# Kernel tuning notes

Hardware: AMD Instinct MI355X
Metric: run time of the kernel (lower is better)

## Reference

```python
import jax, jax.numpy as jnp
from jax import lax
import numpy as np

HEADS = 8
SR = 4  # sr_ratio
LN_EPS = 1e-5


def gaussian_filt(x, kernel_size, sigma):
    # depthwise gaussian blur, x: [B, C, H, W]
    ch = x.shape[1]
    c = jnp.arange(kernel_size, dtype=x.dtype)
    xx = jnp.broadcast_to(c[None, :], (kernel_size, kernel_size))
    yy = xx.T
    mean = (kernel_size - 1) / 2.0
    g = jnp.exp(-((xx - mean) ** 2 + (yy - mean) ** 2) / (2.0 * sigma * sigma))
    g = g / g.sum()  # normalization cancels the 1/(2*pi*var) factor
    kern = jnp.broadcast_to(g[None, None], (ch, 1, kernel_size, kernel_size)).astype(x.dtype)
    p = (kernel_size - 1) // 2
    return lax.conv_general_dilated(
        x, kern, (1, 1), [(p, p), (p, p)],
        dimension_numbers=('NCHW', 'OIHW', 'NCHW'), feature_group_count=ch)


def reconstruct_feature(feature, mask, kernel_size, sigma):
    if kernel_size <= 1:
        return feature
    feature = feature * mask
    out = gaussian_filt(jnp.concatenate([feature, mask], axis=1), kernel_size, sigma)
    f_int = out[:, :-1]
    m_int = out[:, -1:]
    f_int = f_int / (m_int + 1e-6)
    m_bin = (m_int > 0).astype(feature.dtype)
    f_int = f_int * m_bin
    return feature + (1.0 - mask) * f_int


def token2map(x, loc, H, W, kernel_size, sigma):
    # x: [B, N, C], loc: [B, N, 2] in [0,1]
    B, N, C = x.shape
    loc = jnp.clip(loc, 0.0, 1.0) * jnp.array([W - 1, H - 1], dtype=loc.dtype)
    loc = jnp.round(loc).astype(jnp.int32)
    idx = loc[..., 0] + loc[..., 1] * W + (jnp.arange(B, dtype=jnp.int32) * (H * W))[:, None]
    src = jnp.concatenate([x, jnp.ones((B, N, 1), x.dtype)], axis=-1).reshape(B * N, C + 1)
    out = jax.ops.segment_sum(src, idx.reshape(-1), num_segments=B * H * W)
    out = out.reshape(B, H, W, C + 1).transpose(0, 3, 1, 2)  # [B, C+1, H, W]
    feature, mask = out[:, :-1], out[:, -1:]
    feature = feature / (mask + 1e-6)
    mask = (mask > 0).astype(x.dtype)
    feature = feature * mask
    return reconstruct_feature(feature, mask, kernel_size, sigma)


def layer_norm(x, w, b):
    mu = jnp.mean(x, axis=-1, keepdims=True)
    var = jnp.mean((x - mu) ** 2, axis=-1, keepdims=True)
    return (x - mu) * lax.rsqrt(var + LN_EPS) * w + b


def forward(x, x_source, loc_source, conf_source, Wq, Wk, Wv, sr_w, sr_b, ln_w, ln_b, Wp, bp, H, W):
    B, N, C = x.shape
    dh = C // HEADS
    scale = dh ** -0.5
    q = (x @ Wq.T).reshape(B, N, HEADS, dh).transpose(0, 2, 1, 3)  # [B,h,N,dh]
    # token2map + spatial reduction
    xm = token2map(x_source, loc_source, H, W, SR - 1, 2.0)        # [B,C,H,W]
    xs = lax.conv_general_dilated(
        xm, sr_w, (SR, SR), 'VALID',
        dimension_numbers=('NCHW', 'OIHW', 'NCHW')) + sr_b[None, :, None, None]
    xs = xs.reshape(B, C, -1).transpose(0, 2, 1)                   # [B,Ns,C]
    xs = layer_norm(xs, ln_w, ln_b)
    Ns = xs.shape[1]
    k = (xs @ Wk.T).reshape(B, Ns, HEADS, dh).transpose(0, 2, 1, 3)
    v = (xs @ Wv.T).reshape(B, Ns, HEADS, dh).transpose(0, 2, 1, 3)
    attn = jnp.einsum('bhnd,bhmd->bhnm', q, k) * scale             # [B,h,N,Ns]
    attn = attn + conf_source[..., 0][:, None, None, :]            # additive bias
    attn = jax.nn.softmax(attn, axis=-1)
    out = jnp.einsum('bhnm,bhmd->bhnd', attn, v)
    out = out.transpose(0, 2, 1, 3).reshape(B, N, C)
    return out @ Wp.T + bp


def setup_inputs() -> dict:
    key = jax.random.key(0)
    ks = jax.random.split(key, 10)
    B, N, C, Hm = 2, 8192, 256, 128
    Ns = (Hm // SR) * (Hm // SR)
    s = 0.02
    return {
        'x': jax.random.normal(ks[0], (B, N, C), jnp.float32),
        'x_source': jax.random.normal(ks[1], (B, N, C), jnp.float32),
        'loc_source': jax.random.uniform(ks[2], (B, N, 2), jnp.float32),
        'conf_source': jax.random.normal(ks[3], (B, Ns, 1), jnp.float32),
        'Wq': jax.random.normal(ks[4], (C, C), jnp.float32) * s,
        'Wk': jax.random.normal(ks[5], (C, C), jnp.float32) * s,
        'Wv': jax.random.normal(ks[6], (C, C), jnp.float32) * s,
        'sr_w': jax.random.normal(ks[7], (C, C, SR, SR), jnp.float32) * s,
        'sr_b': jnp.zeros((C,), jnp.float32),
        'ln_w': jnp.ones((C,), jnp.float32),
        'ln_b': jnp.zeros((C,), jnp.float32),
        'Wp': jax.random.normal(ks[8], (C, C), jnp.float32) * s,
        'bp': jnp.zeros((C,), jnp.float32),
        'H': Hm,
        'W': Hm,
    }


def reference(x, x_source, loc_source, conf_source, Wq, Wk, Wv, sr_w, sr_b, ln_w, ln_b, Wp, bp, H, W):
    return forward(x, x_source, loc_source, conf_source, Wq, Wk, Wv, sr_w, sr_b, ln_w, ln_b, Wp, bp, H, W)
```

## Files before the change

### kernel.cpp

```cpp
#include <hip/hip_runtime.h>
#include <hip/hip_bf16.h>
#include <cstddef>
#include <cstdint>

#define NTOK 8192
#define CD   256
#define HWPIX 16384
#define WIDTH 128
#define NSEQ 1024

typedef __attribute__((ext_vector_type(8))) short bfrag;
typedef __attribute__((ext_vector_type(4))) float f32x4;
typedef __attribute__((ext_vector_type(4))) unsigned int u32x4;

__device__ inline unsigned short f2bfu(float f) {
    __hip_bfloat16 h = __float2bfloat16(f);
    unsigned short u;
    __builtin_memcpy(&u, &h, 2);
    return u;
}
__device__ inline unsigned int rtn16(float f) {
    unsigned int u = __builtin_bit_cast(unsigned int, f);
    return u + 0x7fffu + ((u >> 16) & 1u);
}
__device__ inline float bits2f(unsigned int u) {
    return __builtin_bit_cast(float, u);
}
__device__ inline void gld16(const unsigned short* g, const unsigned short* l) {
    __builtin_amdgcn_global_load_lds(
        (const __attribute__((address_space(1))) unsigned int*)g,
        (__attribute__((address_space(3))) unsigned int*)l, 16, 0, 0);
}
__device__ inline unsigned int cvtpk(float lo, float hi) {
    unsigned int r;
    asm("v_cvt_pk_bf16_f32 %0, %1, %2" : "=v"(r) : "v"(lo), "v"(hi));
    return r;
}
__device__ inline int kslot(int rin) {
    return (((rin >> 5) * 2 + ((rin >> 2) & 1)) << 4)
         + (((rin >> 3) & 3) << 2) + (rin & 3);
}

__global__ __launch_bounds__(256) void scatter_prep(
        const float* __restrict__ xsrc, const float* __restrict__ loc,
        float* __restrict__ feat, float* __restrict__ maskr,
        const float* __restrict__ srw, const float* __restrict__ Wq,
        const float* __restrict__ Wk, const float* __restrict__ Wv,
        const float* __restrict__ Wp, const float* __restrict__ conf,
        const float* __restrict__ x,
        unsigned short* __restrict__ wTb, unsigned short* __restrict__ wqb,
        unsigned short* __restrict__ wkb, unsigned short* __restrict__ wvb,
        unsigned short* __restrict__ wpb, unsigned short* __restrict__ stg,
        unsigned short* __restrict__ xbf) {
    int gid = blockIdx.x, tid = threadIdx.x;
    if (gid < 16384) {
        int token = gid;
        int b = token >> 13;
        float lx = loc[token * 2 + 0];
        float ly = loc[token * 2 + 1];
        lx = fminf(fmaxf(lx, 0.f), 1.f) * 127.0f;
        ly = fminf(fmaxf(ly, 0.f), 1.f) * 127.0f;
        int ix = __float2int_rn(lx);
        int iy = __float2int_rn(ly);
        int p = b * HWPIX + iy * WIDTH + ix;
        atomicAdd(&feat[(size_t)p * CD + tid], xsrc[(size_t)token * CD + tid]);
        if (tid == 0) atomicAdd(&maskr[p], 1.0f);
    } else if (gid < 20480) {
        int idx = (gid - 16384) * 256 + tid;
        int co = idx >> 12;
        int rest = idx & 4095;
        int k16 = rest >> 8;
        int ci = rest & 255;
        int kh = k16 >> 2, kw = k16 & 3;
        wTb[idx] = f2bfu(srw[(size_t)co * 4096 + ci * 16 + kh * 4 + kw]);
    } else if (gid < 20672) {
        const float* s; unsigned short* d; int base;
        if (gid < 20544)      { s = Wq; d = wqb; base = gid - 20480; }
        else if (gid < 20608) { s = Wk; d = wkb; base = gid - 20544; }
        else                  { s = Wv; d = wvb; base = gid - 20608; }
        int i = (base * 256 + tid) * 4;
        float4 v = *(const float4*)(s + i);
        ushort4 o;
        o.x = f2bfu(v.x); o.y = f2bfu(v.y); o.z = f2bfu(v.z); o.w = f2bfu(v.w);
        *(ushort4*)(d + i) = o;
    } else if (gid < 20928) {
        int n = gid - 20672, t = tid;
        float w = Wp[n * 256 + t];
        unsigned short hu = f2bfu(w);
        float hf = bits2f(((unsigned int)hu) << 16);
        unsigned short lu = f2bfu(w - hf);
        wpb[n * 768 + t]       = hu;
        wpb[n * 768 + 256 + t] = lu;
        wpb[n * 768 + 512 + t] = hu;
    } else if (gid < 20936) {
        int idx = (gid - 20928) * 256 + tid;
        int b = idx >> 10, key = idx & 1023;
        int tile = key >> 6, rin = key & 63;
        int slot = kslot(rin);
        float val = conf[idx] * 1.4426950408889634f;
        #pragma unroll
        for (int h = 0; h < 8; h++)
            *(float*)&stg[((size_t)((b * 8 + h) * 16 + tile)) * 5120
                          + 4864 + slot * 2] = val;
    } else {
        size_t idx = ((size_t)(gid - 20936) * 256 + tid) * 4;
        float4 v = *(const float4*)(x + idx);
        ushort4 o;
        o.x = f2bfu(v.x); o.y = f2bfu(v.y); o.z = f2bfu(v.z); o.w = f2bfu(v.w);
        *(ushort4*)(xbf + idx) = o;
    }
}

__global__ __launch_bounds__(256) void recon_patch(const float* __restrict__ feat,
        const float* __restrict__ maskr, unsigned short* __restrict__ apatch) {
    __shared__ float s_wci[36];
    __shared__ float s_vb[36];
    __shared__ int   s_np[36];
    __shared__ float s_ginv[16];
    __shared__ float s_omb[16];
    int blk = blockIdx.x;
    int b  = blk >> 10;
    int py = (blk >> 5) & 31;
    int px = blk & 31;
    int c = threadIdx.x;
    const float e1 = 0.882496902584595f;
    const float e2 = 0.778800783071405f;
    const float snorm = 1.0f / (1.0f + 4.0f * e1 + 4.0f * e2);
    int y0 = py * 4 - 1, x0 = px * 4 - 1;
    if (c < 36) {
        int ry = c / 6, rx = c % 6;
        int yy = y0 + ry, xx = x0 + rx;
        bool valid = (yy >= 0 && yy <= 127 && xx >= 0 && xx <= 127);
        int yc = min(max(yy, 0), 127), xc = min(max(xx, 0), 127);
        int np_ = b * HWPIX + yc * WIDTH + xc;
        float m = maskr[np_];
        float bin = (m > 0.f) ? 1.f : 0.f;
        float inv = 1.0f / (m + 1e-6f);
        s_wci[c] = valid ? bin * inv : 0.f;
        s_vb[c]  = valid ? bin : 0.f;
        s_np[c]  = np_;
    }
    __syncthreads();
    if (c < 16) {
        int oy = c >> 2, ox = c & 3;
        float gm = 0.f;
        #pragma unroll
        for (int dy = -1; dy <= 1; dy++)
            #pragma unroll
            for (int dx = -1; dx <= 1; dx++) {
                int manh = (dy != 0) + (dx != 0);
                float g = ((manh == 2) ? e2 : (manh == 1) ? e1 : 1.0f) * snorm;
                gm += g * s_vb[(oy + 1 + dy) * 6 + (ox + 1 + dx)];
            }
        s_ginv[c] = (gm > 0.f) ? 1.0f / (gm + 1e-6f) : 0.f;
        s_omb[c]  = 1.0f - s_vb[(oy + 1) * 6 + (ox + 1)];
    }
    float gf[4][4], fcv[4][4];
    #pragma unroll
    for (int oy = 0; oy < 4; oy++)
        #pragma unroll
        for (int ox = 0; ox < 4; ox++) { gf[oy][ox] = 0.f; fcv[oy][ox] = 0.f; }
    #pragma unroll
    for (int ry = 0; ry < 6; ry++) {
        #pragma unroll
        for (int rx = 0; rx < 6; rx++) {
            int j = ry * 6 + rx;
            float f = feat[(size_t)s_np[j] * CD + c] * s_wci[j];
            #pragma unroll
            for (int oy = 0; oy < 4; oy++) {
                int dy = ry - 1 - oy;
                if (dy < -1 || dy > 1) continue;
                #pragma unroll
                for (int ox = 0; ox < 4; ox++) {
                    int dx = rx - 1 - ox;
                    if (dx < -1 || dx > 1) continue;
                    int manh = (dy != 0) + (dx != 0);
                    float g = ((manh == 2) ? e2 : (manh == 1) ? e1 : 1.0f) * snorm;
                    gf[oy][ox] += g * f;
                }
            }
            if (ry >= 1 && ry <= 4 && rx >= 1 && rx <= 4)
                fcv[ry - 1][rx - 1] = f;
        }
    }
    __syncthreads();
    int r = b * 1024 + py * 32 + px;
    size_t base = (size_t)r * 4096 + c;
    #pragma unroll
    for (int oy = 0; oy < 4; oy++)
        #pragma unroll
        for (int ox = 0; ox < 4; ox++) {
            int i = oy * 4 + ox;
            float f_int = gf[oy][ox] * s_ginv[i];
            float res = fcv[oy][ox] + s_omb[i] * f_int;
            apatch[base + (size_t)i * 256] = f2bfu(res);
        }
}

__device__ __forceinline__ void bgemm64_body(
        unsigned short* SB,
        const unsigned short* __restrict__ A,
        const unsigned short* __restrict__ B, const float* __restrict__ bias,
        float* __restrict__ C, unsigned short* __restrict__ dstb,
        int M, int N, int K, int Ka, int kfold, int kSplit, int mode,
        float mult, int bx, int by, int bz) {
    int tid = threadIdx.x;
    int wave = tid >> 6, lane = tid & 63, m15 = lane & 15, quad = lane >> 4;
    int wr = (wave >> 1) * 32, wc = (wave & 1) * 64;
    int m0 = by * 64, n0 = bx * 128;
    int kchunk = K / kSplit, k0 = bz * kchunk;
    int nst = kchunk / 32;
    int srow = tid >> 2, sko = (tid & 3) * 8;
    f32x4 acc[2][4];
    #pragma unroll
    for (int i = 0; i < 2; i++)
        #pragma unroll
        for (int j = 0; j < 4; j++) acc[i][j] = (f32x4){0.f, 0.f, 0.f, 0.f};
    const unsigned short* Ag = A + (size_t)(m0 + srow) * Ka + sko;
    const unsigned short* Bg = B + (size_t)(n0 + srow) * K + k0 + sko;
    #pragma unroll
    for (int pt = 0; pt < 2; pt++) {
        int kl = k0 + pt * 32;
        int ke = (kfold && kl >= kfold) ? kl - kfold : kl;
        unsigned short* l = SB + pt * 6144;
        gld16(Ag + ke, l + wave * 512);
        gld16(Bg + pt * 32, l + 2048 + wave * 512);
        gld16(Bg + (size_t)64 * K + pt * 32, l + 4096 + wave * 512);
    }
    int cur = 0;
    for (int t = 0; t < nst; t++) {
        if (t < nst - 1) asm volatile("s_waitcnt vmcnt(3)" ::: "memory");
        else             asm volatile("s_waitcnt vmcnt(0)" ::: "memory");
        __builtin_amdgcn_s_barrier();
        __builtin_amdgcn_sched_barrier(0);
        const unsigned short* SBc = SB + cur * 6144;
        bfrag af[2], bfr[4];
        #pragma unroll
        for (int mi = 0; mi < 2; mi++)
            af[mi] = *(const bfrag*)&SBc[(wr + mi * 16 + m15) * 32 + quad * 8];
        #pragma unroll
        for (int ni = 0; ni < 4; ni++)
            bfr[ni] = *(const bfrag*)&SBc[2048 + (wc + ni * 16 + m15) * 32
                                          + quad * 8];
        if (t < nst - 2) {
            int nxt = cur + 2; if (nxt >= 3) nxt -= 3;
            int kl = k0 + (t + 2) * 32;
            int ke = (kfold && kl >= kfold) ? kl - kfold : kl;
            unsigned short* l = SB + nxt * 6144;
            gld16(Ag + ke, l + wave * 512);
            gld16(Bg + (t + 2) * 32, l + 2048 + wave * 512);
            gld16(Bg + (size_t)64 * K + (t + 2) * 32, l + 4096 + wave * 512);
        }
        __builtin_amdgcn_s_setprio(1);
        #pragma unroll
        for (int mi = 0; mi < 2; mi++)
            #pragma unroll
            for (int ni = 0; ni < 4; ni++)
                acc[mi][ni] = __builtin_amdgcn_mfma_f32_16x16x32_bf16(
                                  af[mi], bfr[ni], acc[mi][ni], 0, 0, 0);
        __builtin_amdgcn_s_setprio(0);
        cur = (cur == 2) ? 0 : cur + 1;
    }
    if (mode == 2) {
        #pragma unroll
        for (int mi = 0; mi < 2; mi++) {
            #pragma unroll
            for (int i = 0; i < 4; i++) {
                int row = m0 + wr + mi * 16 + quad * 4 + i;
                int b = row >> 13, r = row & 8191;
                #pragma unroll
                for (int ni = 0; ni < 4; ni++) {
                    int col = n0 + wc + ni * 16 + m15;
                    int h = col >> 5, d = col & 31;
                    size_t di = ((((size_t)(b * 8 + h)) << 13) + r) * 32 + d;
                    dstb[di] = f2bfu(acc[mi][ni][i] * mult);
                }
            }
        }
    } else if (mode == 3) {
        #pragma unroll
        for (int mi = 0; mi < 2; mi++) {
            #pragma unroll
            for (int i = 0; i < 4; i++) {
                int row = m0 + wr + mi * 16 + quad * 4 + i;
                int b = row >> 10, key = row & 1023;
                int tile = key >> 6, rin = key & 63;
                int slot = kslot(rin);
                #pragma unroll
                for (int ni = 0; ni < 4; ni++) {
                    int col = n0 + wc + ni * 16 + m15;
                    unsigned short v = f2bfu(acc[mi][ni][i]);
                    if (col < 256) {
                        int h = col >> 5, d = col & 31;
                        size_t di = ((size_t)((b * 8 + h) * 16 + tile)) * 5120
                                    + slot * 40 + d;
                        dstb[di] = v;
                    } else {
                        int c2 = col - 256;
                        int h = c2 >> 5, d = c2 & 31;
                        size_t di = ((size_t)((b * 8 + h) * 16 + tile)) * 5120
                                    + 2560 + d * 72 + rin;
                        dstb[di] = v;
                    }
                }
            }
        }
    } else if (mode == 4) {
        #pragma unroll
        for (int mi = 0; mi < 2; mi++) {
            #pragma unroll
            for (int i = 0; i < 4; i++) {
                size_t row = ((size_t)bz * M + m0 + wr + mi * 16 + quad * 4 + i) * N;
                #pragma unroll
                for (int ni = 0; ni < 4; ni++) {
                    int col = n0 + wc + ni * 16 + m15;
                    C[row + col] = acc[mi][ni][i];
                }
            }
        }
    } else {
        #pragma unroll
        for (int mi = 0; mi < 2; mi++) {
            #pragma unroll
            for (int i = 0; i < 4; i++) {
                size_t row = (size_t)(m0 + wr + mi * 16 + quad * 4 + i) * N;
                #pragma unroll
                for (int ni = 0; ni < 4; ni++) {
                    int col = n0 + wc + ni * 16 + m15;
                    C[row + col] = acc[mi][ni][i] + (bias ? bias[col] : 0.f);
                }
            }
        }
    }
}

__global__ __launch_bounds__(256) void bgemm64(const unsigned short* A,
        const unsigned short* B, const float* bias,
        float* C, unsigned short* dstb,
        int M, int N, int K, int Ka, int kfold, int kSplit, int mode,
        float mult) {
    __shared__ __align__(16) unsigned short SB[3 * 6144];
    bgemm64_body(SB, A, B, bias, C, dstb, M, N, K, Ka, kfold, kSplit,
                 mode, mult, blockIdx.x, blockIdx.y, blockIdx.z);
}

__global__ __launch_bounds__(256) void qkv_fused(const unsigned short* xbf,
        const unsigned short* wqb, const unsigned short* xsbf,
        const unsigned short* wkb, unsigned short* Qbf,
        unsigned short* stg, float SC) {
    __shared__ __align__(16) unsigned short SB[3 * 6144];
    int g = blockIdx.x;
    if (g < 512) {
        bgemm64_body(SB, xbf, wqb, nullptr, nullptr, Qbf,
                     16384, 256, 256, 256, 0, 1, 2, SC, g & 1, g >> 1, 0);
    } else {
        int g2 = g - 512;
        bgemm64_body(SB, xsbf, wkb, nullptr, nullptr, stg,
                     2048, 512, 256, 256, 0, 1, 3, 1.f, g2 & 3, g2 >> 2, 0);
    }
}

__global__ __launch_bounds__(256) void ln_red(const float* __restrict__ part,
        const float* __restrict__ srb, const float* __restrict__ w,
        const float* __restrict__ bvec, unsigned short* __restrict__ outb) {
    int row = blockIdx.x;
    int c = threadIdx.x;
    float v = srb[c];
    #pragma unroll
    for (int z = 0; z < 8; z++)
        v += part[((size_t)z * 2048 + row) * 256 + c];
    __shared__ float red[4];
    float s = v;
    #pragma unroll
    for (int o = 32; o >= 1; o >>= 1) s += __shfl_down(s, o, 64);
    if ((c & 63) == 0) red[c >> 6] = s;
    __syncthreads();
    float mean = (red[0] + red[1] + red[2] + red[3]) * (1.f / 256.f);
    __syncthreads();
    float d = v - mean;
    float s2 = d * d;
    #pragma unroll
    for (int o = 32; o >= 1; o >>= 1) s2 += __shfl_down(s2, o, 64);
    if ((c & 63) == 0) red[c >> 6] = s2;
    __syncthreads();
    float var = (red[0] + red[1] + red[2] + red[3]) * (1.f / 256.f);
    float r = 1.0f / sqrtf(var + 1e-5f);
    outb[(size_t)row * 256 + c] = f2bfu(d * r * w[c] + bvec[c]);
}

__global__ __launch_bounds__(256, 2) void attn_v13(
        const unsigned short* __restrict__ Qb,
        const unsigned short* __restrict__ STG,
        unsigned short* __restrict__ aout) {
    __shared__ __align__(16) unsigned short SB[3][5120];
    int tid  = threadIdx.x;
    int wave = tid >> 6;
    int lane = tid & 63;
    int m15  = lane & 15;
    int quad = lane >> 4;
    int flat = blockIdx.y * 32 + blockIdx.x;
    int j  = flat >> 3;
    int bh = (flat & 7) + ((j >> 5) << 3);
    int b  = bh >> 3;
    int h  = bh & 7;
    int qbase = (j & 31) * 256 + wave * 64;

    const unsigned short* qp = Qb + ((size_t)bh * NTOK + qbase) * 32;
    bfrag Qa[4];
    #pragma unroll
    for (int tq = 0; tq < 4; tq++)
        Qa[tq] = *(const bfrag*)(qp + (tq * 16 + m15) * 32 + quad * 8);
    const unsigned short* sg = STG + (size_t)bh * 16 * 5120;

    bfrag ones;
    #pragma unroll
    for (int i = 0; i < 8; i++) ones[i] = (short)0x3F80;

    f32x4 O[4][2];
    f32x4 Lac[4];
    #pragma unroll
    for (int tq = 0; tq < 4; tq++) {
        O[tq][0] = (f32x4){0.f, 0.f, 0.f, 0.f};
        O[tq][1] = (f32x4){0.f, 0.f, 0.f, 0.f};
        Lac[tq]  = (f32x4){0.f, 0.f, 0.f, 0.f};
    }

    #pragma unroll
    for (int pt = 0; pt < 2; pt++) {
        const unsigned short* g = sg + (size_t)pt * 5120;
        unsigned short* l = &SB[pt][0];
        gld16(g + wave * 512 + lane * 8, l + wave * 512);
        gld16(g + (wave + 4) * 512 + lane * 8, l + (wave + 4) * 512);
        if (wave < 2) gld16(g + (8 + wave) * 512 + lane * 8, l + (8 + wave) * 512);
    }

    int cur = 0;
    for (int t = 0; t < 16; t++) {
        if (t < 15) {
            if (wave < 2) asm volatile("s_waitcnt vmcnt(3)" ::: "memory");
            else          asm volatile("s_waitcnt vmcnt(2)" ::: "memory");
        } else {
            asm volatile("s_waitcnt vmcnt(0)" ::: "memory");
        }
        __builtin_amdgcn_s_barrier();
        __builtin_amdgcn_sched_barrier(0);
        const unsigned short* Ks = &SB[0][0] + cur * 5120;
        const unsigned short* Vs = Ks + 2560;
        const float* Cf = (const float*)(Ks + 4864);
        bfrag kf[4]; f32x4 ccf[4];
        #pragma unroll
        for (int s = 0; s < 4; s++) {
            kf[s]  = *(const bfrag*)&Ks[(s * 16 + m15) * 40 + quad * 8];
            ccf[s] = *(const f32x4*)&Cf[s * 16 + quad * 4];
        }
        if (t < 14) {
            int nxt = cur + 2; if (nxt >= 3) nxt -= 3;
            const unsigned short* g = sg + (size_t)(t + 2) * 5120;
            unsigned short* l = &SB[0][0] + nxt * 5120;
            gld16(g + wave * 512 + lane * 8, l + wave * 512);
            gld16(g + (wave + 4) * 512 + lane * 8, l + (wave + 4) * 512);
            if (wave < 2) gld16(g + (8 + wave) * 512 + lane * 8,
                                l + (8 + wave) * 512);
        }
        bfrag Pb[4][2];
        #pragma unroll
        for (int tq = 0; tq < 4; tq++) {
            f32x4 S[4];
            __builtin_amdgcn_s_setprio(1);
            #pragma unroll
            for (int s = 0; s < 4; s++)
                S[s] = __builtin_amdgcn_mfma_f32_16x16x32_bf16(kf[s], Qa[tq],
                                                               ccf[s], 0, 0, 0);
            __builtin_amdgcn_s_setprio(0);
            float v[4][4];
            #pragma unroll
            for (int s = 0; s < 4; s++)
                #pragma unroll
                for (int r = 0; r < 4; r++)
                    v[s][r] = __builtin_amdgcn_exp2f(S[s][r]);
            #pragma unroll
            for (int k2 = 0; k2 < 2; k2++) {
                u32x4 pw;
                pw[0] = cvtpk(v[2 * k2][0],     v[2 * k2][1]);
                pw[1] = cvtpk(v[2 * k2][2],     v[2 * k2][3]);
                pw[2] = cvtpk(v[2 * k2 + 1][0], v[2 * k2 + 1][1]);
                pw[3] = cvtpk(v[2 * k2 + 1][2], v[2 * k2 + 1][3]);
                Pb[tq][k2] = __builtin_bit_cast(bfrag, pw);
            }
        }
        bfrag vfr[2][2];
        #pragma unroll
        for (int k2 = 0; k2 < 2; k2++)
            #pragma unroll
            for (int dt = 0; dt < 2; dt++)
                vfr[k2][dt] = *(const bfrag*)&Vs[(dt * 16 + m15) * 72 +
                                                 k2 * 32 + quad * 8];
        __builtin_amdgcn_s_setprio(1);
        #pragma unroll
        for (int k2 = 0; k2 < 2; k2++)
            #pragma unroll
            for (int tq = 0; tq < 4; tq++) {
                #pragma unroll
                for (int dt = 0; dt < 2; dt++)
                    O[tq][dt] = __builtin_amdgcn_mfma_f32_16x16x32_bf16(
                                    Pb[tq][k2], vfr[k2][dt], O[tq][dt], 0, 0, 0);
                Lac[tq] = __builtin_amdgcn_mfma_f32_16x16x32_bf16(
                                    Pb[tq][k2], ones, Lac[tq], 0, 0, 0);
            }
        __builtin_amdgcn_s_setprio(0);
        cur = (cur == 2) ? 0 : cur + 1;
    }
    #pragma unroll
    for (int tq = 0; tq < 4; tq++) {
        #pragma unroll
        for (int r = 0; r < 4; r++) {
            float inv = 1.0f / Lac[tq][r];
            int row = b * NTOK + qbase + tq * 16 + quad * 4 + r;
            size_t rb = (size_t)row * 512;
            #pragma unroll
            for (int dt = 0; dt < 2; dt++) {
                float o = O[tq][dt][r] * inv;
                unsigned int hr = rtn16(o);
                unsigned short hu = hr >> 16;
                float hf = bits2f(hr & 0xffff0000u);
                unsigned short lu = rtn16(o - hf) >> 16;
                int col = h * 32 + dt * 16 + m15;
                aout[rb + col]       = hu;
                aout[rb + 256 + col] = lu;
            }
        }
    }
}

extern "C" void kernel_launch(void* const* d_in, const int* in_sizes, int n_in,
                              void* d_out, int out_size, void* d_ws, size_t ws_size,
                              hipStream_t stream) {
    const float* x        = (const float*)d_in[0];
    const float* x_source = (const float*)d_in[1];
    const float* loc      = (const float*)d_in[2];
    const float* conf     = (const float*)d_in[3];
    const float* Wq       = (const float*)d_in[4];
    const float* Wk       = (const float*)d_in[5];
    const float* Wv       = (const float*)d_in[6];
    const float* srw      = (const float*)d_in[7];
    const float* srb      = (const float*)d_in[8];
    const float* lnw      = (const float*)d_in[9];
    const float* lnb      = (const float*)d_in[10];
    const float* Wp       = (const float*)d_in[11];
    const float* bp       = (const float*)d_in[12];
    float* out = (float*)d_out;
    float* ws  = (float*)d_ws;

    float* feat = ws;
    unsigned short* Qbf = (unsigned short*)ws;
    float* maskr = ws + 8388608;
    unsigned short* apatch = (unsigned short*)(ws + 8421376);
    unsigned short* aouts  = (unsigned short*)(ws + 8421376);
    unsigned short* wTb    = (unsigned short*)(ws + 12615680);
    unsigned short* stg  = (unsigned short*)(ws + 14712832);
    unsigned short* wqb  = (unsigned short*)(ws + 15368192);
    unsigned short* wkb  = (unsigned short*)(ws + 15400960);
    unsigned short* wvb  = (unsigned short*)(ws + 15433728);
    unsigned short* wpb  = (unsigned short*)(ws + 15466496);
    unsigned short* xsbf = (unsigned short*)(ws + 16089088);
    unsigned short* xbf  = (unsigned short*)(ws + 16351232);
    float*          part = ws + 18448384;

    const float SC = 0.17677669529663687f * 1.4426950408889634f;

    hipMemsetAsync(feat, 0, (size_t)(8388608 + 32768) * sizeof(float), stream);

    scatter_prep<<<25032, 256, 0, stream>>>(x_source, loc, feat, maskr,
                                            srw, Wq, Wk, Wv, Wp, conf, x,
                                            wTb, wqb, wkb, wvb, wpb, stg, xbf);
    recon_patch<<<2048, 256, 0, stream>>>(feat, maskr, apatch);
    bgemm64<<<dim3(2, 32, 8), 256, 0, stream>>>(apatch, wTb, nullptr,
                                                part, nullptr,
                                                2048, 256, 4096, 4096, 0,
                                                8, 4, 1.f);
    ln_red<<<2048, 256, 0, stream>>>(part, srb, lnw, lnb, xsbf);
    qkv_fused<<<640, 256, 0, stream>>>(xbf, wqb, xsbf, wkb, Qbf, stg, SC);
    attn_v13<<<dim3(32, 16), 256, 0, stream>>>(Qbf, stg, aouts);
    bgemm64<<<dim3(2, 256, 1), 256, 0, stream>>>(aouts, wpb, bp,
                                                 out, nullptr,
                                                 16384, 256, 768, 512, 256,
                                                 1, 0, 1.f);
}
```

Measured before the change: 210.9 us.

## Fuse Q projection GEMM into recon_patch launch, run KV GEMM separately

Moves the Q projection GEMM, which depends only on x, into the same launch as the patch reconstruction, so the two independent workloads share one grid and fill the GPU together. The KV projection now runs as its own bgemm64 launch after the layer norm. Because feat is still live while Q is written, Qbf moves to a separate workspace region instead of aliasing feat. Recon's shared memory is carved out of the GEMM's shared buffer, which raises that block type's LDS footprint and may reduce occupancy for recon blocks.

Result: no change. 213.8 us (+1.4%).

```diff
diff --git a/kernel.cpp b/kernel.cpp
--- a/kernel.cpp
+++ b/kernel.cpp
@@ -111,14 +111,14 @@
     }
 }
 
-__global__ __launch_bounds__(256) void recon_patch(const float* __restrict__ feat,
-        const float* __restrict__ maskr, unsigned short* __restrict__ apatch) {
-    __shared__ float s_wci[36];
-    __shared__ float s_vb[36];
-    __shared__ int   s_np[36];
-    __shared__ float s_ginv[16];
-    __shared__ float s_omb[16];
-    int blk = blockIdx.x;
+__device__ __forceinline__ void recon_body(unsigned short* SBraw,
+        const float* __restrict__ feat, const float* __restrict__ maskr,
+        unsigned short* __restrict__ apatch, int blk) {
+    float* s_wci  = (float*)SBraw;
+    float* s_vb   = s_wci + 36;
+    float* s_ginv = s_vb + 36;
+    float* s_omb  = s_ginv + 16;
+    int*   s_np   = (int*)(s_omb + 16);
     int b  = blk >> 10;
     int py = (blk >> 5) & 31;
     int px = blk & 31;
@@ -344,19 +344,20 @@
                  mode, mult, blockIdx.x, blockIdx.y, blockIdx.z);
 }
 
-__global__ __launch_bounds__(256) void qkv_fused(const unsigned short* xbf,
-        const unsigned short* wqb, const unsigned short* xsbf,
-        const unsigned short* wkb, unsigned short* Qbf,
-        unsigned short* stg, float SC) {
+__global__ __launch_bounds__(256) void recon_q(
+        const float* __restrict__ feat, const float* __restrict__ maskr,
+        unsigned short* __restrict__ apatch,
+        const unsigned short* __restrict__ xbf,
+        const unsigned short* __restrict__ wqb,
+        unsigned short* __restrict__ Qbf, float SC) {
     __shared__ __align__(16) unsigned short SB[3 * 6144];
     int g = blockIdx.x;
-    if (g < 512) {
+    if (g < 2048) {
+        recon_body(SB, feat, maskr, apatch, g);
+    } else {
+        int g2 = g - 2048;
         bgemm64_body(SB, xbf, wqb, nullptr, nullptr, Qbf,
-                     16384, 256, 256, 256, 0, 1, 2, SC, g & 1, g >> 1, 0);
-    } else {
-        int g2 = g - 512;
-        bgemm64_body(SB, xsbf, wkb, nullptr, nullptr, stg,
-                     2048, 512, 256, 256, 0, 1, 3, 1.f, g2 & 3, g2 >> 2, 0);
+                     16384, 256, 256, 256, 0, 1, 2, SC, g2 & 1, g2 >> 1, 0);
     }
 }
 
@@ -552,7 +553,6 @@
     float* ws  = (float*)d_ws;
 
     float* feat = ws;
-    unsigned short* Qbf = (unsigned short*)ws;
     float* maskr = ws + 8388608;
     unsigned short* apatch = (unsigned short*)(ws + 8421376);
     unsigned short* aouts  = (unsigned short*)(ws + 8421376);
@@ -565,6 +565,7 @@
     unsigned short* xsbf = (unsigned short*)(ws + 16089088);
     unsigned short* xbf  = (unsigned short*)(ws + 16351232);
     float*          part = ws + 18448384;
+    unsigned short* Qbf  = (unsigned short*)(ws + 22642688);
 
     const float SC = 0.17677669529663687f * 1.4426950408889634f;
 
@@ -573,13 +574,16 @@
     scatter_prep<<<25032, 256, 0, stream>>>(x_source, loc, feat, maskr,
                                             srw, Wq, Wk, Wv, Wp, conf, x,
                                             wTb, wqb, wkb, wvb, wpb, stg, xbf);
-    recon_patch<<<2048, 256, 0, stream>>>(feat, maskr, apatch);
+    recon_q<<<2560, 256, 0, stream>>>(feat, maskr, apatch, xbf, wqb, Qbf, SC);
     bgemm64<<<dim3(2, 32, 8), 256, 0, stream>>>(apatch, wTb, nullptr,
                                                 part, nullptr,
                                                 2048, 256, 4096, 4096, 0,
                                                 8, 4, 1.f);
     ln_red<<<2048, 256, 0, stream>>>(part, srb, lnw, lnb, xsbf);
-    qkv_fused<<<640, 256, 0, stream>>>(xbf, wqb, xsbf, wkb, Qbf, stg, SC);
+    bgemm64<<<dim3(4, 32, 1), 256, 0, stream>>>(xsbf, wkb, nullptr,
+                                                nullptr, stg,
+                                                2048, 512, 256, 256, 0,
+                                                1, 3, 1.f);
     attn_v13<<<dim3(32, 16), 256, 0, stream>>>(Qbf, stg, aouts);
     bgemm64<<<dim3(2, 256, 1), 256, 0, stream>>>(aouts, wpb, bp,
                                                  out, nullptr,
```
